# Optimization experiments

Hardware: AMD Instinct MI355X
Metric: run time of the kernel (lower is better)

## Reference

```python
import jax, jax.numpy as jnp
import numpy as np

D_MODEL = 512; D_STATE = 64; D_CONV = 4; EXPAND = 2; HEADDIM = 64
D_INNER = EXPAND * D_MODEL          # 1024
NHEADS = D_INNER // HEADDIM         # 16
D_IN_PROJ = 2 * D_INNER + 2 * D_STATE + NHEADS  # z, xBC, dt
CONV_DIM = D_INNER + 2 * D_STATE
BETA = 0.5
BATCH = 8; SEQLEN = 1024
EPS_LN = 1e-12; EPS_RMS = 1e-5


def layernorm(x, w, b, eps=EPS_LN):
    mu = jnp.mean(x, axis=-1, keepdims=True)
    var = jnp.var(x, axis=-1, keepdims=True)
    return (x - mu) * jax.lax.rsqrt(var + eps) * w + b


def causal_dw_conv(x, w, b):
    # x: (b, l, c); w: (c, d_conv) depthwise; causal left-pad d_conv-1
    xt = jnp.transpose(x, (0, 2, 1))                 # (b, c, l)
    k = w[:, None, :]                                # (c, 1, d_conv)
    y = jax.lax.conv_general_dilated(
        xt, k, window_strides=(1,), padding=[(D_CONV - 1, 0)],
        feature_group_count=CONV_DIM,
        dimension_numbers=('NCH', 'OIH', 'NCH'))
    return jnp.transpose(y, (0, 2, 1)) + b


def ssd(x, dt, A, Bm, Cm, Dp):
    # x: (b,l,h,p)  dt: (b,l,h)  A: (h)  Bm,Cm: (b,l,n)  Dp: (h)
    dA = jnp.exp(dt * A)  # (b,l,h) decay per step

    def step(h, inp):
        dA_t, dt_t, B_t, C_t, x_t = inp
        # h: (b, heads, p, n)
        h = h * dA_t[:, :, None, None] + jnp.einsum('bh,bn,bhp->bhpn', dt_t, B_t, x_t)
        y = jnp.einsum('bhpn,bn->bhp', h, C_t)
        return h, y

    init = jnp.zeros((x.shape[0], NHEADS, HEADDIM, D_STATE), x.dtype)
    xs = (jnp.moveaxis(dA, 1, 0), jnp.moveaxis(dt, 1, 0),
          jnp.moveaxis(Bm, 1, 0), jnp.moveaxis(Cm, 1, 0), jnp.moveaxis(x, 1, 0))
    _, ys = jax.lax.scan(step, init, xs)
    y = jnp.moveaxis(ys, 0, 1)           # (b,l,h,p)
    return y + x * Dp[None, None, :, None]


def mamba2(u, in_proj_w, conv_w, conv_b, dt_bias, A_log, Dp, norm_w, out_proj_w):
    zxbcdt = u @ in_proj_w.T                                   # (b,l,D_IN_PROJ)
    z, xBC, dt = jnp.split(zxbcdt, [D_INNER, D_INNER + CONV_DIM], axis=-1)
    dt = jax.nn.softplus(dt + dt_bias)                          # (b,l,h)
    xBC = jax.nn.silu(causal_dw_conv(xBC, conv_w, conv_b))
    x, Bm, Cm = jnp.split(xBC, [D_INNER, D_INNER + D_STATE], axis=-1)
    x = x.reshape(x.shape[0], x.shape[1], NHEADS, HEADDIM)
    A = -jnp.exp(A_log)
    y = ssd(x, dt, A, Bm, Cm, Dp)
    y = y.reshape(y.shape[0], y.shape[1], D_INNER)
    g = y * jax.nn.silu(z)                                      # gated RMSNorm
    g = g * jax.lax.rsqrt(jnp.mean(g * g, axis=-1, keepdims=True) + EPS_RMS) * norm_w
    return g @ out_proj_w.T


def ffn(x, w1, b1, w2, b2, lnw, lnb):
    h = jax.nn.gelu(x @ w1.T + b1, approximate=False)
    h = h @ w2.T + b2
    return layernorm(h + x, lnw, lnb)


def setup_inputs() -> dict:
    key = jax.random.key(0)
    ks = jax.random.split(key, 12)
    item_emb = jax.random.normal(ks[0], (BATCH, SEQLEN, D_MODEL), jnp.float32)
    item_idx = jnp.zeros((BATCH, SEQLEN), jnp.int32)          # single sequence per row
    flip_index = jnp.arange(SEQLEN - 1, -1, -1, dtype=jnp.int64)
    s = 0.02
    in_proj_w = jax.random.normal(ks[1], (D_IN_PROJ, D_MODEL), jnp.float32) * s
    conv_w = jax.random.uniform(ks[2], (CONV_DIM, D_CONV), jnp.float32, -0.5, 0.5)
    conv_b = jnp.zeros((CONV_DIM,), jnp.float32)
    # dt_bias = inverse softplus of dt ~ U[1e-3, 0.1] in log space (mamba init)
    dt = jnp.exp(jax.random.uniform(ks[3], (NHEADS,), jnp.float32,
                                    np.log(1e-3), np.log(0.1)))
    dt_bias = dt + jnp.log(-jnp.expm1(-dt))
    A_log = jnp.log(jax.random.uniform(ks[4], (NHEADS,), jnp.float32, 1.0, 16.0))
    Dp = jnp.ones((NHEADS,), jnp.float32)
    norm_w = jnp.ones((D_INNER,), jnp.float32)
    out_proj_w = jax.random.normal(ks[5], (D_MODEL, D_INNER), jnp.float32) * s
    ln_w = jnp.ones((D_MODEL,), jnp.float32); ln_b = jnp.zeros((D_MODEL,), jnp.float32)
    ffn_w1 = jax.random.normal(ks[6], (4 * D_MODEL, D_MODEL), jnp.float32) * s
    ffn_b1 = jnp.zeros((4 * D_MODEL,), jnp.float32)
    ffn_w2 = jax.random.normal(ks[7], (D_MODEL, 4 * D_MODEL), jnp.float32) * s
    ffn_b2 = jnp.zeros((D_MODEL,), jnp.float32)
    ffn_ln_w = jnp.ones((D_MODEL,), jnp.float32); ffn_ln_b = jnp.zeros((D_MODEL,), jnp.float32)
    return dict(item_emb=item_emb, item_idx=item_idx, flip_index=flip_index,
                in_proj_w=in_proj_w, conv_w=conv_w, conv_b=conv_b, dt_bias=dt_bias,
                A_log=A_log, Dp=Dp, norm_w=norm_w, out_proj_w=out_proj_w,
                ln_w=ln_w, ln_b=ln_b, ffn_w1=ffn_w1, ffn_b1=ffn_b1,
                ffn_w2=ffn_w2, ffn_b2=ffn_b2, ffn_ln_w=ffn_ln_w, ffn_ln_b=ffn_ln_b)


def reference(item_emb, item_idx, flip_index, in_proj_w, conv_w, conv_b, dt_bias,
              A_log, Dp, norm_w, out_proj_w, ln_w, ln_b,
              ffn_w1, ffn_b1, ffn_w2, ffn_b2, ffn_ln_w, ffn_ln_b):
    # item_idx (seq_idx) is all-zeros -> no state resets; dropout is eval-mode identity.
    params = (in_proj_w, conv_w, conv_b, dt_bias, A_log, Dp, norm_w, out_proj_w)
    fwd = mamba2(item_emb, *params)
    bwd = mamba2(item_emb[:, flip_index, :], *params)   # shared weights, as in source
    h = fwd + bwd * BETA + item_emb
    h = layernorm(h, ln_w, ln_b)
    return ffn(h, ffn_w1, ffn_b1, ffn_w2, ffn_b2, ffn_ln_w, ffn_ln_b)
```

## Files before the change

### kernel.cpp

```cpp
#include <hip/hip_runtime.h>
#include <math.h>

#define SEQ     1024
#define NBATCH  8
#define NTOK    8192
#define DMODEL  512
#define DINNER  1024
#define NHEADS  16
#define DPROJ   2192
#define DPROJP  2304
#define CONVDIM 1152
#define DFFN    2048

typedef short bf16x8 __attribute__((ext_vector_type(8)));
typedef float f32x4  __attribute__((ext_vector_type(4)));

__device__ inline unsigned short f2bf(float f) {
  union { float f; unsigned int u; } v; v.f = f;
  unsigned int u = v.u;
  return (unsigned short)((u + 0x7FFFu + ((u >> 16) & 1u)) >> 16);
}
__device__ inline float bf2f(unsigned short s) {
  union { unsigned int u; float f; } v; v.u = ((unsigned int)s) << 16;
  return v.f;
}

__device__ inline float fexp(float x) { return __expf(x); }
__device__ inline float frcp(float x) { return __builtin_amdgcn_rcpf(x); }
__device__ inline float silu_f(float v) { return v * frcp(1.f + fexp(-v)); }
__device__ inline float gelu_f(float v) {
  float x = v * 0.7071067811865476f;
  float ax = fabsf(x);
  float t = frcp(1.f + 0.3275911f * ax);
  float p = ((((1.061405429f * t - 1.453152027f) * t + 1.421413741f) * t
              - 0.284496736f) * t + 0.254829592f) * t;
  float er = copysignf(1.f - p * fexp(-ax * ax), x);
  return 0.5f * v * (1.f + er);
}

__device__ inline int xcd_swz(int flat, int nwg) {
  return (flat & 7) * (nwg >> 3) + (flat >> 3);
}

#define GLDS16(g, l)                                                         \
  __builtin_amdgcn_global_load_lds(                                          \
      (const __attribute__((address_space(1))) unsigned int*)(g),            \
      (__attribute__((address_space(3))) unsigned int*)(l), 16, 0, 0)

__global__ __launch_bounds__(256)
void cvt_all(const float* __restrict__ u, const float* __restrict__ inw,
             const float* __restrict__ outw, const float* __restrict__ w1,
             const float* __restrict__ w2,
             unsigned short* __restrict__ u_bf, unsigned short* __restrict__ winb,
             unsigned short* __restrict__ woutb, unsigned short* __restrict__ w1b,
             unsigned short* __restrict__ w2b) {
  int i = blockIdx.x * 256 + threadIdx.x;
  const int nu = NTOK * DMODEL;
  const int n0 = DPROJP * DMODEL;
  const int n1 = DMODEL * DINNER;
  const int n2 = DFFN * DMODEL;
  const int n3 = DMODEL * DFFN;
  if (i < nu) {
    u_bf[i] = f2bf(u[i]);
  } else if ((i -= nu) < n0) {
    int r = i / DMODEL;
    winb[i] = (r < DPROJ) ? f2bf(inw[i]) : (unsigned short)0;
  } else if ((i -= n0) < n1) {
    woutb[i] = f2bf(outw[i]);
  } else if ((i -= n1) < n2) {
    w1b[i] = f2bf(w1[i]);
  } else if ((i -= n2) < n3) {
    w2b[i] = f2bf(w2[i]);
  }
}

template <int MODE>
__global__ __launch_bounds__(256)
void gemm_bt(const unsigned short* __restrict__ A, const unsigned short* __restrict__ B,
             void* __restrict__ Cout, const float* __restrict__ bias,
             float* __restrict__ aux, int Ksub, int lda, int Nreal, size_t zstrideC) {
  __shared__ unsigned short sA[2][128 * 32];
  __shared__ unsigned short sB[2][128 * 32];
  const int tid = threadIdx.x;
  const int nwg = gridDim.x * gridDim.y * gridDim.z;
  const int flat = blockIdx.x + gridDim.x * (blockIdx.y + gridDim.y * blockIdx.z);
  const int swz = xcd_swz(flat, nwg);
  const int bx = swz % gridDim.x;
  const int tmp = swz / gridDim.x;
  const int by = tmp % gridDim.y;
  const int bz = tmp / gridDim.y;
  const int lane = tid & 63;
  const int wave = tid >> 6;
  const int wm = wave >> 1, wn = wave & 1;
  const int arow = tid >> 2;
  const int acol = (tid & 3) << 3;

  const unsigned short* pA = A + (size_t)(by * 128 + arow) * lda + bz * Ksub + acol;
  const unsigned short* pB = B + (size_t)(bx * 128 + arow) * lda + bz * Ksub + acol;
  const size_t stride64 = (size_t)64 * lda;
  char* sAw[2] = { (char*)&sA[0][0] + wave * 1024, (char*)&sA[1][0] + wave * 1024 };
  char* sBw[2] = { (char*)&sB[0][0] + wave * 1024, (char*)&sB[1][0] + wave * 1024 };

  f32x4 acc[4][4];
#pragma unroll
  for (int i = 0; i < 4; i++)
#pragma unroll
    for (int j = 0; j < 4; j++) { f32x4 z = {0.f, 0.f, 0.f, 0.f}; acc[i][j] = z; }

  GLDS16(pA, sAw[0]);
  GLDS16(pA + stride64, sAw[0] + 4096);
  GLDS16(pB, sBw[0]);
  GLDS16(pB + stride64, sBw[0] + 4096);
  pA += 32; pB += 32;
  __syncthreads();

  const int lrow = lane & 15;
  const int lkq = (lane >> 4) << 3;
  int cur = 0;
  for (int k0 = 0; k0 < Ksub; k0 += 32) {
    if (k0 + 32 < Ksub) {
      const int nxt = cur ^ 1;
      GLDS16(pA, sAw[nxt]);
      GLDS16(pA + stride64, sAw[nxt] + 4096);
      GLDS16(pB, sBw[nxt]);
      GLDS16(pB + stride64, sBw[nxt] + 4096);
      pA += 32; pB += 32;
    }
    bf16x8 af[4], bfr[4];
#pragma unroll
    for (int mi = 0; mi < 4; mi++)
      af[mi] = *(const bf16x8*)&sA[cur][(wm * 64 + mi * 16 + lrow) * 32 + lkq];
#pragma unroll
    for (int ni = 0; ni < 4; ni++)
      bfr[ni] = *(const bf16x8*)&sB[cur][(wn * 64 + ni * 16 + lrow) * 32 + lkq];
#pragma unroll
    for (int mi = 0; mi < 4; mi++)
#pragma unroll
      for (int ni = 0; ni < 4; ni++)
        acc[mi][ni] = __builtin_amdgcn_mfma_f32_16x16x32_bf16(af[mi], bfr[ni], acc[mi][ni], 0, 0, 0);
    __syncthreads();
    cur ^= 1;
  }

  const int row0 = by * 128 + wm * 64;
  const int col0 = bx * 128 + wn * 64;
  float* outf = (float*)Cout;
  unsigned short* outp16 = (unsigned short*)Cout + (size_t)bz * zstrideC;
#pragma unroll
  for (int mi = 0; mi < 4; mi++) {
#pragma unroll
    for (int ni = 0; ni < 4; ni++) {
      const int col = col0 + ni * 16 + lrow;
      if (col < Nreal) {
        const float bval = (MODE == 0 || MODE == 1) && bias ? bias[col] : 0.f;
#pragma unroll
        for (int r = 0; r < 4; r++) {
          const int row = row0 + mi * 16 + ((lane >> 4) << 2) + r;
          float v = acc[mi][ni][r] + bval;
          if (MODE == 1) {
            ((unsigned short*)Cout)[(size_t)row * Nreal + col] = f2bf(gelu_f(v));
          } else if (MODE == 2) {
            ((unsigned short*)Cout)[(size_t)row * Nreal + col] = f2bf(v);
            if (col >= 2176) aux[(size_t)row * 16 + (col - 2176)] = v;
          } else if (MODE == 3) {
            outp16[(size_t)row * Nreal + col] = f2bf(v);
          } else {
            outf[(size_t)row * Nreal + col] = v;
          }
        }
      }
    }
  }
}

__global__ __launch_bounds__(256)
void dt_conv_bc(const float* __restrict__ zdt, const float* __restrict__ dt_bias,
                float* __restrict__ dtf, float* __restrict__ dtb,
                const unsigned short* __restrict__ zxb, const float* __restrict__ cw,
                const float* __restrict__ cb,
                unsigned short* __restrict__ xbcf, unsigned short* __restrict__ xbcb) {
  const int tid = threadIdx.x;
  if (blockIdx.x < 1024) {
    int i = blockIdx.x * 256 + tid;
    int dir = i >> 17;
    int rem = i & 131071;
    int row = rem >> 10;
    int t = rem & 1023;
    int b = row >> 4, h = row & 15;
    int srow = (b << 10) + (dir ? (1023 - t) : t);
    float v = zdt[(size_t)srow * 16 + h] + dt_bias[h];
    float dt = (v > 20.f) ? v : log1pf(fexp(v));
    (dir ? dtb : dtf)[(row << 10) + t] = dt;
    return;
  }
  const int bid = blockIdx.x - 1024;
  const int sx = bid & 15, b = bid >> 4;
  const int c128 = tid & 127;
  const int c = 1024 + c128;
  const int seg = sx * 2 + (tid >> 7);
  const int t0 = seg << 5;
  const float w0 = cw[c * 4 + 0], w1 = cw[c * 4 + 1], w2 = cw[c * 4 + 2], w3 = cw[c * 4 + 3];
  const float bias = cb[c];
  const unsigned short* src = zxb + (size_t)(b << 10) * DPROJ + DINNER + c;
  unsigned short* dstf = xbcf + (size_t)(b << 10) * 128 + c128;
  unsigned short* dstb = xbcb + (size_t)(b << 10) * 128 + c128;
  float r0 = 0.f, r1 = 0.f, r2 = 0.f;
  if (t0 >= 3) {
    r0 = bf2f(src[(size_t)(t0 - 3) * DPROJ]);
    r1 = bf2f(src[(size_t)(t0 - 2) * DPROJ]);
    r2 = bf2f(src[(size_t)(t0 - 1) * DPROJ]);
  }
  for (int s = t0; s < t0 + 32; s++) {
    float x = bf2f(src[(size_t)s * DPROJ]);
    float vf = bias + w0 * r0 + w1 * r1 + w2 * r2 + w3 * x;
    dstf[(size_t)s * 128] = f2bf(silu_f(vf));
    int tp = 1026 - s;
    if (tp <= 1023) {
      float vb = bias + w0 * x + w1 * r2 + w2 * r1 + w3 * r0;
      dstb[(size_t)tp * 128] = f2bf(silu_f(vb));
    }
    r0 = r1; r1 = r2; r2 = x;
  }
  if (seg == 31) {
    float v2 = bias + w1 * r2 + w2 * r1 + w3 * r0;
    float v1 = bias + w2 * r2 + w3 * r1;
    float v0 = bias + w3 * r2;
    dstb[(size_t)2 * 128] = f2bf(silu_f(v2));
    dstb[(size_t)1 * 128] = f2bf(silu_f(v1));
    dstb[0] = f2bf(silu_f(v0));
  }
}

__global__ __launch_bounds__(512)
void ssd_chunk(const unsigned short* __restrict__ zxb,
               const unsigned short* __restrict__ xbcf, const unsigned short* __restrict__ xbcb,
               const float* __restrict__ cw, const float* __restrict__ cb,
               const float* __restrict__ dtf, const float* __restrict__ dtb,
               const float* __restrict__ A_log, const float* __restrict__ Dp,
               unsigned short* __restrict__ yf, unsigned short* __restrict__ yb) {
  const int blk = xcd_swz(blockIdx.x, 256);
  const int dir = blk >> 7;
  const int b = (blk >> 4) & 7;
  const int h = blk & 15;
  const unsigned short* xbc = dir ? xbcb : xbcf;
  const float* dts = (dir ? dtb : dtf) + ((size_t)((b << 4) + h) << 10);
  unsigned short* yo = dir ? yb : yf;
  const float A = -expf(A_log[h]);
  const float Dh = Dp[h];
  const int tid = threadIdx.x;
  const int lane = tid & 63;
  const int w = tid >> 6;
  const int wm = w >> 1;
  const int wn = w & 1;
  const int lrow = lane & 15;
  const int quad = lane >> 4;
  const int lk8 = quad << 3;
  const int bS = b << 10;

  __shared__ unsigned short Cb[2][64 * 72];
  __shared__ unsigned short Bb[2][64 * 72];
  __shared__ unsigned short Xt[2][64 * 72];
  __shared__ unsigned short Bt[2][64 * 72];
  __shared__ unsigned short Hb[2][64 * 72];
  __shared__ unsigned short Mb[64 * 72];
  __shared__ float sdt_all[1024];
  __shared__ float Lv_all[16][64];
  __shared__ float ev_all[16][64];
  __shared__ float wv_all[16][64];
  __shared__ float dtot_all[16];

  const unsigned short* bcrow = xbc + (size_t)(bS + (tid >> 3)) * 128 + (tid & 7) * 8;
  const int pr = tid & 31;
  const int sg = tid >> 5;
  const int ccx = h * 64 + pr * 2;
  const unsigned short* bvrow = xbc + (size_t)(bS + sg * 4) * 128 + pr * 2;
  const float4 wx0 = *(const float4*)(cw + ccx * 4);
  const float4 wx1 = *(const float4*)(cw + (ccx + 1) * 4);
  const float bx0 = cb[ccx], bx1 = cb[ccx + 1];

  uint4 vb, vc;
  unsigned int bv[4];
  unsigned int xin[7];

  auto stage_load = [&](int c) {
    const unsigned short* rp = bcrow + (size_t)c * 64 * 128;
    vb = *(const uint4*)(rp);
    vc = *(const uint4*)(rp + 64);
    const unsigned short* tp = bvrow + (size_t)c * 64 * 128;
#pragma unroll
    for (int k = 0; k < 4; k++) bv[k] = *(const unsigned int*)(tp + (size_t)k * 128);
    const int li0 = c * 64 + sg * 4 - 3;
#pragma unroll
    for (int j = 0; j < 7; j++) {
      const int li = li0 + j;
      const int g = dir ? (1023 - li) : li;
      xin[j] = (g >= 0 && g < 1024)
               ? *(const unsigned int*)(zxb + (size_t)(bS + g) * DPROJ + DINNER + ccx)
               : 0u;
    }
  };

  auto stage_write = [&](int buf, int c) {
    *(uint4*)&Bb[buf][(tid >> 3) * 72 + (tid & 7) * 8] = vb;
    *(uint4*)&Cb[buf][(tid >> 3) * 72 + (tid & 7) * 8] = vc;
    float f0[7], f1[7];
#pragma unroll
    for (int j = 0; j < 7; j++) {
      f0[j] = bf2f((unsigned short)(xin[j] & 0xffff));
      f1[j] = bf2f((unsigned short)(xin[j] >> 16));
    }
    unsigned short x0[4], x1[4], b0[4], b1[4];
#pragma unroll
    for (int k = 0; k < 4; k++) {
      const float ws = wv_all[c][sg * 4 + k];
      float v0 = bx0 + wx0.x * f0[k] + wx0.y * f0[k + 1] + wx0.z * f0[k + 2] + wx0.w * f0[k + 3];
      float v1 = bx1 + wx1.x * f1[k] + wx1.y * f1[k + 1] + wx1.z * f1[k + 2] + wx1.w * f1[k + 3];
      x0[k] = f2bf(silu_f(v0));
      x1[k] = f2bf(silu_f(v1));
      b0[k] = f2bf(bf2f((unsigned short)(bv[k] & 0xffff)) * ws);
      b1[k] = f2bf(bf2f((unsigned short)(bv[k] >> 16)) * ws);
    }
    *(uint2*)&Xt[buf][(pr * 2 + 0) * 72 + sg * 4] = *(const uint2*)x0;
    *(uint2*)&Xt[buf][(pr * 2 + 1) * 72 + sg * 4] = *(const uint2*)x1;
    *(uint2*)&Bt[buf][(pr * 2 + 0) * 72 + sg * 4] = *(const uint2*)b0;
    *(uint2*)&Bt[buf][(pr * 2 + 1) * 72 + sg * 4] = *(const uint2*)b1;
  };

  stage_load(0);

  *(float2*)&sdt_all[tid * 2] = *(const float2*)(dts + tid * 2);
  {
    uint4 z; z.x = 0u; z.y = 0u; z.z = 0u; z.w = 0u;
    *(uint4*)&Hb[0][(tid >> 3) * 72 + (tid & 7) * 8] = z;
  }
  __syncthreads();

#pragma unroll
  for (int r = 0; r < 2; r++) {
    const int c = w * 2 + r;
    float dtl = sdt_all[c * 64 + lane];
    float v = dtl;
#pragma unroll
    for (int off = 1; off < 64; off <<= 1) {
      float o = __shfl_up(v, off);
      if (lane >= off) v += o;
    }
    const float Lv = A * v;
    const float LL = __shfl(Lv, 63);
    Lv_all[c][lane] = Lv;
    ev_all[c][lane] = fexp(Lv);
    wv_all[c][lane] = dtl * fexp(LL - Lv);
    if (lane == 0) dtot_all[c] = fexp(LL);
  }
  __syncthreads();

  stage_write(0, 0);
  stage_load(1);
  __syncthreads();

  f32x4 hacc[2];
#pragma unroll
  for (int j = 0; j < 2; j++) { f32x4 z = {0.f, 0.f, 0.f, 0.f}; hacc[j] = z; }

  int cur = 0;
  for (int c = 0; c < 16; c++) {
    const int t0 = c << 6;

    f32x4 m1[2];
#pragma unroll
    for (int j = 0; j < 2; j++) { f32x4 z = {0.f, 0.f, 0.f, 0.f}; m1[j] = z; }
#pragma unroll
    for (int kq = 0; kq < 2; kq++) {
      bf16x8 af = *(const bf16x8*)&Cb[cur][(wm * 16 + lrow) * 72 + kq * 32 + lk8];
#pragma unroll
      for (int j = 0; j < 2; j++) {
        bf16x8 bf = *(const bf16x8*)&Bb[cur][(wn * 32 + j * 16 + lrow) * 72 + kq * 32 + lk8];
        m1[j] = __builtin_amdgcn_mfma_f32_16x16x32_bf16(af, bf, m1[j], 0, 0, 0);
      }
    }
#pragma unroll
    for (int r = 0; r < 4; r++) {
      const int i = wm * 16 + quad * 4 + r;
      const float Li = Lv_all[c][i];
#pragma unroll
      for (int j = 0; j < 2; j++) {
        const int s = wn * 32 + j * 16 + lrow;
        const float Ls = Lv_all[c][s];
        const float ds = sdt_all[c * 64 + s];
        float val = (s <= i) ? m1[j][r] * fexp(Li - Ls) * ds : 0.f;
        Mb[i * 72 + s] = f2bf(val);
      }
    }
    __syncthreads();

    f32x4 Y[2], T[2], S[2];
#pragma unroll
    for (int j = 0; j < 2; j++) {
      f32x4 z = {0.f, 0.f, 0.f, 0.f};
      Y[j] = z; T[j] = z; S[j] = z;
    }
#pragma unroll
    for (int kq = 0; kq < 2; kq++) {
      bf16x8 am = *(const bf16x8*)&Mb[(wm * 16 + lrow) * 72 + kq * 32 + lk8];
      bf16x8 ac = *(const bf16x8*)&Cb[cur][(wm * 16 + lrow) * 72 + kq * 32 + lk8];
      bf16x8 ax = *(const bf16x8*)&Xt[cur][(wm * 16 + lrow) * 72 + kq * 32 + lk8];
#pragma unroll
      for (int j = 0; j < 2; j++) {
        const int brow = (wn * 32 + j * 16 + lrow) * 72 + kq * 32 + lk8;
        bf16x8 bx = *(const bf16x8*)&Xt[cur][brow];
        bf16x8 bh = *(const bf16x8*)&Hb[cur][brow];
        bf16x8 bw = *(const bf16x8*)&Bt[cur][brow];
        Y[j] = __builtin_amdgcn_mfma_f32_16x16x32_bf16(am, bx, Y[j], 0, 0, 0);
        T[j] = __builtin_amdgcn_mfma_f32_16x16x32_bf16(ac, bh, T[j], 0, 0, 0);
        S[j] = __builtin_amdgcn_mfma_f32_16x16x32_bf16(ax, bw, S[j], 0, 0, 0);
      }
    }

    const float dtot = dtot_all[c];
#pragma unroll
    for (int r = 0; r < 4; r++) {
      const int i = wm * 16 + quad * 4 + r;
      const float ei = ev_all[c][i];
#pragma unroll
      for (int j = 0; j < 2; j++) {
        const int p = wn * 32 + j * 16 + lrow;
        float yv = Y[j][r] + ei * T[j][r] + Dh * bf2f(Xt[cur][p * 72 + i]);
        yo[(size_t)(bS + t0 + i) * DINNER + h * 64 + p] = f2bf(yv);
      }
    }
#pragma unroll
    for (int j = 0; j < 2; j++)
#pragma unroll
      for (int r = 0; r < 4; r++)
        hacc[j][r] = dtot * hacc[j][r] + S[j][r];

    const int nxt = cur ^ 1;
    if (c + 1 < 16) {
#pragma unroll
      for (int j = 0; j < 2; j++)
#pragma unroll
        for (int r = 0; r < 4; r++)
          Hb[nxt][(wm * 16 + quad * 4 + r) * 72 + wn * 32 + j * 16 + lrow] = f2bf(hacc[j][r]);
      stage_write(nxt, c + 1);
      if (c + 2 < 16) stage_load(c + 2);
    }
    __syncthreads();
    cur = nxt;
  }
}

__device__ inline float2 block_sum2_256(float a, float b) {
#pragma unroll
  for (int o = 32; o >= 1; o >>= 1) { a += __shfl_xor(a, o); b += __shfl_xor(b, o); }
  __shared__ float ra[4], rb[4];
  const int lane = threadIdx.x & 63, w = threadIdx.x >> 6;
  if (lane == 0) { ra[w] = a; rb[w] = b; }
  __syncthreads();
  float2 out;
  out.x = ra[0] + ra[1] + ra[2] + ra[3];
  out.y = rb[0] + rb[1] + rb[2] + rb[3];
  return out;
}

__global__ __launch_bounds__(256)
void gate_rms_comb(const unsigned short* __restrict__ yf, const unsigned short* __restrict__ yb,
                   const unsigned short* __restrict__ zxb, const float* __restrict__ nw,
                   unsigned short* __restrict__ comb) {
  const int bt = blockIdx.x;
  const int b = bt >> 10, t = bt & 1023;
  const int zrowb = (b << 10) + (1023 - t);
  const int tid = threadIdx.x;
  ushort4 yf4 = *(const ushort4*)(yf + (size_t)bt * DINNER + tid * 4);
  ushort4 yb4 = *(const ushort4*)(yb + (size_t)bt * DINNER + tid * 4);
  ushort4 zf4 = *(const ushort4*)(zxb + (size_t)bt * DPROJ + tid * 4);
  ushort4 zb4 = *(const ushort4*)(zxb + (size_t)zrowb * DPROJ + tid * 4);
  float gf[4], gb[4];
  gf[0] = bf2f(yf4.x) * silu_f(bf2f(zf4.x));
  gf[1] = bf2f(yf4.y) * silu_f(bf2f(zf4.y));
  gf[2] = bf2f(yf4.z) * silu_f(bf2f(zf4.z));
  gf[3] = bf2f(yf4.w) * silu_f(bf2f(zf4.w));
  gb[0] = bf2f(yb4.x) * silu_f(bf2f(zb4.x));
  gb[1] = bf2f(yb4.y) * silu_f(bf2f(zb4.y));
  gb[2] = bf2f(yb4.z) * silu_f(bf2f(zb4.z));
  gb[3] = bf2f(yb4.w) * silu_f(bf2f(zb4.w));
  float2 sr = block_sum2_256(gf[0]*gf[0] + gf[1]*gf[1] + gf[2]*gf[2] + gf[3]*gf[3],
                             gb[0]*gb[0] + gb[1]*gb[1] + gb[2]*gb[2] + gb[3]*gb[3]);
  float sf = rsqrtf(sr.x * (1.f / 1024.f) + 1e-5f);
  float sb = 0.5f * rsqrtf(sr.y * (1.f / 1024.f) + 1e-5f);
  float4 wv = *(const float4*)(nw + tid * 4);
  unsigned short* o = comb + (size_t)bt * DINNER + tid * 4;
  o[0] = f2bf((gf[0] * sf + gb[0] * sb) * wv.x);
  o[1] = f2bf((gf[1] * sf + gb[1] * sb) * wv.y);
  o[2] = f2bf((gf[2] * sf + gb[2] * sb) * wv.z);
  o[3] = f2bf((gf[3] * sf + gb[3] * sb) * wv.w);
}

__global__ __launch_bounds__(256)
void combine_ln(const unsigned short* __restrict__ mo, const float* __restrict__ u,
                const float* __restrict__ w, const float* __restrict__ bias,
                float* __restrict__ hln, unsigned short* __restrict__ hbf) {
  const int bt = blockIdx.x;
  const int tid = threadIdx.x;
  const float2 uu = *(const float2*)(u + (size_t)bt * DMODEL + tid * 2);
  float vx = uu.x, vy = uu.y;
#pragma unroll
  for (int z = 0; z < 2; z++) {
    ushort2 p = *(const ushort2*)(mo + (size_t)z * NTOK * DMODEL + (size_t)bt * DMODEL + tid * 2);
    vx += bf2f(p.x);
    vy += bf2f(p.y);
  }
  float2 sr = block_sum2_256(vx + vy, vx * vx + vy * vy);
  float mean = sr.x * (1.f / 512.f);
  float var = sr.y * (1.f / 512.f) - mean * mean;
  float inv = rsqrtf(var + 1e-12f);
  float2 wv = *(const float2*)(w + tid * 2);
  float2 bv = *(const float2*)(bias + tid * 2);
  float ox = (vx - mean) * inv * wv.x + bv.x;
  float oy = (vy - mean) * inv * wv.y + bv.y;
  *(float2*)(hln + (size_t)bt * DMODEL + tid * 2) = make_float2(ox, oy);
  hbf[(size_t)bt * DMODEL + tid * 2] = f2bf(ox);
  hbf[(size_t)bt * DMODEL + tid * 2 + 1] = f2bf(oy);
}

__global__ __launch_bounds__(256)
void final_ln(const unsigned short* __restrict__ f2, const float* __restrict__ b2,
              const float* __restrict__ hln,
              const float* __restrict__ w, const float* __restrict__ bias,
              float* __restrict__ outp) {
  const int bt = blockIdx.x;
  const int tid = threadIdx.x;
  const float2 bb = *(const float2*)(b2 + tid * 2);
  const float2 h = *(const float2*)(hln + (size_t)bt * DMODEL + tid * 2);
  float vx = bb.x + h.x;
  float vy = bb.y + h.y;
#pragma unroll
  for (int z = 0; z < 2; z++) {
    ushort2 p = *(const ushort2*)(f2 + (size_t)z * NTOK * DMODEL + (size_t)bt * DMODEL + tid * 2);
    vx += bf2f(p.x);
    vy += bf2f(p.y);
  }
  float2 sr = block_sum2_256(vx + vy, vx * vx + vy * vy);
  float mean = sr.x * (1.f / 512.f);
  float var = sr.y * (1.f / 512.f) - mean * mean;
  float inv = rsqrtf(var + 1e-12f);
  float2 wv = *(const float2*)(w + tid * 2);
  float2 bv = *(const float2*)(bias + tid * 2);
  *(float2*)(outp + (size_t)bt * DMODEL + tid * 2) =
      make_float2((vx - mean) * inv * wv.x + bv.x, (vy - mean) * inv * wv.y + bv.y);
}

extern "C" void kernel_launch(void* const* d_in, const int* in_sizes, int n_in,
                              void* d_out, int out_size, void* d_ws, size_t ws_size,
                              hipStream_t stream) {
  const float* item_emb   = (const float*)d_in[0];
  const float* in_proj_w  = (const float*)d_in[3];
  const float* conv_w     = (const float*)d_in[4];
  const float* conv_b     = (const float*)d_in[5];
  const float* dt_bias    = (const float*)d_in[6];
  const float* A_log      = (const float*)d_in[7];
  const float* Dp         = (const float*)d_in[8];
  const float* norm_w     = (const float*)d_in[9];
  const float* out_proj_w = (const float*)d_in[10];
  const float* ln_w       = (const float*)d_in[11];
  const float* ln_b       = (const float*)d_in[12];
  const float* w1         = (const float*)d_in[13];
  const float* b1         = (const float*)d_in[14];
  const float* w2         = (const float*)d_in[15];
  const float* b2         = (const float*)d_in[16];
  const float* fln_w      = (const float*)d_in[17];
  const float* fln_b      = (const float*)d_in[18];
  float* outp = (float*)d_out;
  char* ws = (char*)d_ws;

  const size_t o_ubf  = 0;
  const size_t o_win  = 8388608;
  const size_t o_wout = 10747904;
  const size_t o_w1   = 11796480;
  const size_t o_w2   = 13893632;
  const size_t o_dtf  = 15990784;
  const size_t o_dtb  = 16515072;
  const size_t o_zdt  = 17039360;
  const size_t o_zxb  = 17563648;
  const size_t o_xcf  = 53477376;
  const size_t o_xbcf = 72351744;
  const size_t o_xbcb = 74448896;
  const size_t o_yf   = 91226112;
  const size_t o_yb   = 108003328;
  const size_t o_comb = o_xcf;
  const size_t o_mo   = o_zxb;
  const size_t o_hln  = o_yb;
  const size_t o_hbf  = o_ubf;
  const size_t o_h1   = o_xbcf;
  const size_t o_f2   = o_zxb;

  unsigned short* u_bf  = (unsigned short*)(ws + o_ubf);
  unsigned short* winb  = (unsigned short*)(ws + o_win);
  unsigned short* woutb = (unsigned short*)(ws + o_wout);
  unsigned short* w1b   = (unsigned short*)(ws + o_w1);
  unsigned short* w2b   = (unsigned short*)(ws + o_w2);
  float* dtf = (float*)(ws + o_dtf);
  float* dtb = (float*)(ws + o_dtb);
  float* zdt = (float*)(ws + o_zdt);
  unsigned short* zxb  = (unsigned short*)(ws + o_zxb);
  unsigned short* xbcf = (unsigned short*)(ws + o_xbcf);
  unsigned short* xbcb = (unsigned short*)(ws + o_xbcb);
  unsigned short* yf  = (unsigned short*)(ws + o_yf);
  unsigned short* yb  = (unsigned short*)(ws + o_yb);
  unsigned short* comb = (unsigned short*)(ws + o_comb);
  unsigned short* mo  = (unsigned short*)(ws + o_mo);
  float* hln = (float*)(ws + o_hln);
  unsigned short* hbf = (unsigned short*)(ws + o_hbf);
  unsigned short* h1b = (unsigned short*)(ws + o_h1);
  unsigned short* f2  = (unsigned short*)(ws + o_f2);

  {
    int n = NTOK * DMODEL + DPROJP * DMODEL + DMODEL * DINNER + DFFN * DMODEL + DMODEL * DFFN;
    cvt_all<<<(n + 255) / 256, 256, 0, stream>>>(item_emb, in_proj_w, out_proj_w, w1, w2,
                                                 u_bf, winb, woutb, w1b, w2b);
  }

  gemm_bt<2><<<dim3(DPROJP / 128, NTOK / 128), 256, 0, stream>>>(
      u_bf, winb, zxb, nullptr, zdt, DMODEL, DMODEL, DPROJ, 0);

  dt_conv_bc<<<1152, 256, 0, stream>>>(zdt, dt_bias, dtf, dtb,
                                       zxb, conv_w, conv_b, xbcf, xbcb);

  ssd_chunk<<<256, 512, 0, stream>>>(zxb, xbcf, xbcb, conv_w, conv_b,
                                     dtf, dtb, A_log, Dp, yf, yb);

  gate_rms_comb<<<NTOK, 256, 0, stream>>>(yf, yb, zxb, norm_w, comb);

  gemm_bt<3><<<dim3(DMODEL / 128, NTOK / 128, 2), 256, 0, stream>>>(
      comb, woutb, mo, nullptr, nullptr, DINNER / 2, DINNER, DMODEL,
      (size_t)NTOK * DMODEL);

  combine_ln<<<NTOK, 256, 0, stream>>>(mo, item_emb, ln_w, ln_b, hln, hbf);

  gemm_bt<1><<<dim3(DFFN / 128, NTOK / 128), 256, 0, stream>>>(
      hbf, w1b, h1b, b1, nullptr, DMODEL, DMODEL, DFFN, 0);

  gemm_bt<3><<<dim3(DMODEL / 128, NTOK / 128, 2), 256, 0, stream>>>(
      h1b, w2b, f2, nullptr, nullptr, DFFN / 2, DFFN, DMODEL,
      (size_t)NTOK * DMODEL);

  final_ln<<<NTOK, 256, 0, stream>>>(f2, b2, hln, fln_w, fln_b, outp);

  (void)in_sizes; (void)n_in; (void)out_size; (void)ws_size;
}
```

Measured before the change: 320.8 us.

## Split SSD chunk kernel across headdim halves and load C/B fragments directly

Each (direction, batch, head) unit is now split into two blocks, one per 32-wide half of the head dimension, which doubles the grid to 512 blocks. The launch bounds request 4 blocks per CU so more work runs at once on the sequential chunk scan. The C and B MFMA fragments are now read straight from global memory into registers instead of being staged through shared memory. This shrinks shared memory use and removes some LDS traffic. In exchange, the C·B^T intra-chunk matrix and the per-chunk dt cumsum/B-weighting work are computed twice for each head, and the global fragment loads may add latency.

```diff
diff --git a/kernel.cpp b/kernel.cpp
--- a/kernel.cpp
+++ b/kernel.cpp
@@ -231,17 +231,19 @@
   }
 }
 
-__global__ __launch_bounds__(512)
+__global__ __launch_bounds__(512, 4)
 void ssd_chunk(const unsigned short* __restrict__ zxb,
                const unsigned short* __restrict__ xbcf, const unsigned short* __restrict__ xbcb,
                const float* __restrict__ cw, const float* __restrict__ cb,
                const float* __restrict__ dtf, const float* __restrict__ dtb,
                const float* __restrict__ A_log, const float* __restrict__ Dp,
                unsigned short* __restrict__ yf, unsigned short* __restrict__ yb) {
-  const int blk = xcd_swz(blockIdx.x, 256);
-  const int dir = blk >> 7;
-  const int b = (blk >> 4) & 7;
-  const int h = blk & 15;
+  const int blk = xcd_swz(blockIdx.x, 512);
+  const int ph = blk & 1;
+  const int unit = blk >> 1;
+  const int dir = unit >> 7;
+  const int b = (unit >> 4) & 7;
+  const int h = unit & 15;
   const unsigned short* xbc = dir ? xbcb : xbcf;
   const float* dts = (dir ? dtb : dtf) + ((size_t)((b << 4) + h) << 10);
   unsigned short* yo = dir ? yb : yf;
@@ -250,18 +252,16 @@
   const int tid = threadIdx.x;
   const int lane = tid & 63;
   const int w = tid >> 6;
-  const int wm = w >> 1;
-  const int wn = w & 1;
+  const int iw = w >> 1;
+  const int sw = w & 1;
   const int lrow = lane & 15;
   const int quad = lane >> 4;
   const int lk8 = quad << 3;
   const int bS = b << 10;
 
-  __shared__ unsigned short Cb[2][64 * 72];
-  __shared__ unsigned short Bb[2][64 * 72];
-  __shared__ unsigned short Xt[2][64 * 72];
+  __shared__ unsigned short Xt[2][32 * 72];
   __shared__ unsigned short Bt[2][64 * 72];
-  __shared__ unsigned short Hb[2][64 * 72];
+  __shared__ unsigned short Hb[2][32 * 72];
   __shared__ unsigned short Mb[64 * 72];
   __shared__ float sdt_all[1024];
   __shared__ float Lv_all[16][64];
@@ -269,29 +269,38 @@
   __shared__ float wv_all[16][64];
   __shared__ float dtot_all[16];
 
-  const unsigned short* bcrow = xbc + (size_t)(bS + (tid >> 3)) * 128 + (tid & 7) * 8;
   const int pr = tid & 31;
   const int sg = tid >> 5;
-  const int ccx = h * 64 + pr * 2;
   const unsigned short* bvrow = xbc + (size_t)(bS + sg * 4) * 128 + pr * 2;
+  const int pr2 = tid & 15;
+  const int sg2 = tid >> 4;
+  const int ccx = h * 64 + ph * 32 + pr2 * 2;
   const float4 wx0 = *(const float4*)(cw + ccx * 4);
   const float4 wx1 = *(const float4*)(cw + (ccx + 1) * 4);
   const float bx0 = cb[ccx], bx1 = cb[ccx + 1];
 
-  uint4 vb, vc;
   unsigned int bv[4];
-  unsigned int xin[7];
-
+  unsigned int xin[5];
+  bf16x8 af[2], bfr[4];
+
+  auto frag_load = [&](int c) {
+    const unsigned short* base = xbc + (size_t)(bS + c * 64) * 128;
+#pragma unroll
+    for (int kq = 0; kq < 2; kq++) {
+      af[kq] = *(const bf16x8*)(base + (size_t)(iw * 16 + lrow) * 128 + 64 + kq * 32 + lk8);
+#pragma unroll
+      for (int j = 0; j < 2; j++)
+        bfr[j * 2 + kq] =
+            *(const bf16x8*)(base + (size_t)(sw * 32 + j * 16 + lrow) * 128 + kq * 32 + lk8);
+    }
+  };
   auto stage_load = [&](int c) {
-    const unsigned short* rp = bcrow + (size_t)c * 64 * 128;
-    vb = *(const uint4*)(rp);
-    vc = *(const uint4*)(rp + 64);
     const unsigned short* tp = bvrow + (size_t)c * 64 * 128;
 #pragma unroll
     for (int k = 0; k < 4; k++) bv[k] = *(const unsigned int*)(tp + (size_t)k * 128);
-    const int li0 = c * 64 + sg * 4 - 3;
-#pragma unroll
-    for (int j = 0; j < 7; j++) {
+    const int li0 = c * 64 + sg2 * 2 - 3;
+#pragma unroll
+    for (int j = 0; j < 5; j++) {
       const int li = li0 + j;
       const int g = dir ? (1023 - li) : li;
       xin[j] = (g >= 0 && g < 1024)
@@ -299,39 +308,41 @@
                : 0u;
     }
   };
-
   auto stage_write = [&](int buf, int c) {
-    *(uint4*)&Bb[buf][(tid >> 3) * 72 + (tid & 7) * 8] = vb;
-    *(uint4*)&Cb[buf][(tid >> 3) * 72 + (tid & 7) * 8] = vc;
-    float f0[7], f1[7];
-#pragma unroll
-    for (int j = 0; j < 7; j++) {
+    unsigned short b0[4], b1[4];
+#pragma unroll
+    for (int k = 0; k < 4; k++) {
+      const float ws = wv_all[c][sg * 4 + k];
+      b0[k] = f2bf(bf2f((unsigned short)(bv[k] & 0xffff)) * ws);
+      b1[k] = f2bf(bf2f((unsigned short)(bv[k] >> 16)) * ws);
+    }
+    *(uint2*)&Bt[buf][(pr * 2 + 0) * 72 + sg * 4] = *(const uint2*)b0;
+    *(uint2*)&Bt[buf][(pr * 2 + 1) * 72 + sg * 4] = *(const uint2*)b1;
+    float f0[5], f1[5];
+#pragma unroll
+    for (int j = 0; j < 5; j++) {
       f0[j] = bf2f((unsigned short)(xin[j] & 0xffff));
       f1[j] = bf2f((unsigned short)(xin[j] >> 16));
     }
-    unsigned short x0[4], x1[4], b0[4], b1[4];
-#pragma unroll
-    for (int k = 0; k < 4; k++) {
-      const float ws = wv_all[c][sg * 4 + k];
+    unsigned short x0[2], x1[2];
+#pragma unroll
+    for (int k = 0; k < 2; k++) {
       float v0 = bx0 + wx0.x * f0[k] + wx0.y * f0[k + 1] + wx0.z * f0[k + 2] + wx0.w * f0[k + 3];
       float v1 = bx1 + wx1.x * f1[k] + wx1.y * f1[k + 1] + wx1.z * f1[k + 2] + wx1.w * f1[k + 3];
       x0[k] = f2bf(silu_f(v0));
       x1[k] = f2bf(silu_f(v1));
-      b0[k] = f2bf(bf2f((unsigned short)(bv[k] & 0xffff)) * ws);
-      b1[k] = f2bf(bf2f((unsigned short)(bv[k] >> 16)) * ws);
-    }
-    *(uint2*)&Xt[buf][(pr * 2 + 0) * 72 + sg * 4] = *(const uint2*)x0;
-    *(uint2*)&Xt[buf][(pr * 2 + 1) * 72 + sg * 4] = *(const uint2*)x1;
-    *(uint2*)&Bt[buf][(pr * 2 + 0) * 72 + sg * 4] = *(const uint2*)b0;
-    *(uint2*)&Bt[buf][(pr * 2 + 1) * 72 + sg * 4] = *(const uint2*)b1;
+    }
+    *(unsigned int*)&Xt[buf][(pr2 * 2 + 0) * 72 + sg2 * 2] = *(const unsigned int*)x0;
+    *(unsigned int*)&Xt[buf][(pr2 * 2 + 1) * 72 + sg2 * 2] = *(const unsigned int*)x1;
   };
 
+  frag_load(0);
   stage_load(0);
 
   *(float2*)&sdt_all[tid * 2] = *(const float2*)(dts + tid * 2);
-  {
+  if (tid < 288) {
     uint4 z; z.x = 0u; z.y = 0u; z.z = 0u; z.w = 0u;
-    *(uint4*)&Hb[0][(tid >> 3) * 72 + (tid & 7) * 8] = z;
+    *(uint4*)&Hb[0][tid * 8] = z;
   }
   __syncthreads();
 
@@ -358,9 +369,7 @@
   stage_load(1);
   __syncthreads();
 
-  f32x4 hacc[2];
-#pragma unroll
-  for (int j = 0; j < 2; j++) { f32x4 z = {0.f, 0.f, 0.f, 0.f}; hacc[j] = z; }
+  f32x4 hacc = {0.f, 0.f, 0.f, 0.f};
 
   int cur = 0;
   for (int c = 0; c < 16; c++) {
@@ -370,21 +379,17 @@
 #pragma unroll
     for (int j = 0; j < 2; j++) { f32x4 z = {0.f, 0.f, 0.f, 0.f}; m1[j] = z; }
 #pragma unroll
-    for (int kq = 0; kq < 2; kq++) {
-      bf16x8 af = *(const bf16x8*)&Cb[cur][(wm * 16 + lrow) * 72 + kq * 32 + lk8];
+    for (int kq = 0; kq < 2; kq++)
+#pragma unroll
+      for (int j = 0; j < 2; j++)
+        m1[j] = __builtin_amdgcn_mfma_f32_16x16x32_bf16(af[kq], bfr[j * 2 + kq], m1[j], 0, 0, 0);
+#pragma unroll
+    for (int r = 0; r < 4; r++) {
+      const int i = iw * 16 + quad * 4 + r;
+      const float Li = Lv_all[c][i];
 #pragma unroll
       for (int j = 0; j < 2; j++) {
-        bf16x8 bf = *(const bf16x8*)&Bb[cur][(wn * 32 + j * 16 + lrow) * 72 + kq * 32 + lk8];
-        m1[j] = __builtin_amdgcn_mfma_f32_16x16x32_bf16(af, bf, m1[j], 0, 0, 0);
-      }
-    }
-#pragma unroll
-    for (int r = 0; r < 4; r++) {
-      const int i = wm * 16 + quad * 4 + r;
-      const float Li = Lv_all[c][i];
-#pragma unroll
-      for (int j = 0; j < 2; j++) {
-        const int s = wn * 32 + j * 16 + lrow;
+        const int s = sw * 32 + j * 16 + lrow;
         const float Ls = Lv_all[c][s];
         const float ds = sdt_all[c * 64 + s];
         float val = (s <= i) ? m1[j][r] * fexp(Li - Ls) * ds : 0.f;
@@ -393,56 +398,45 @@
     }
     __syncthreads();
 
-    f32x4 Y[2], T[2], S[2];
-#pragma unroll
-    for (int j = 0; j < 2; j++) {
-      f32x4 z = {0.f, 0.f, 0.f, 0.f};
-      Y[j] = z; T[j] = z; S[j] = z;
-    }
+    f32x4 Y = {0.f, 0.f, 0.f, 0.f};
+    f32x4 T = {0.f, 0.f, 0.f, 0.f};
+    f32x4 S = {0.f, 0.f, 0.f, 0.f};
+    bf16x8 am[2], xp[2];
 #pragma unroll
     for (int kq = 0; kq < 2; kq++) {
-      bf16x8 am = *(const bf16x8*)&Mb[(wm * 16 + lrow) * 72 + kq * 32 + lk8];
-      bf16x8 ac = *(const bf16x8*)&Cb[cur][(wm * 16 + lrow) * 72 + kq * 32 + lk8];
-      bf16x8 ax = *(const bf16x8*)&Xt[cur][(wm * 16 + lrow) * 72 + kq * 32 + lk8];
-#pragma unroll
-      for (int j = 0; j < 2; j++) {
-        const int brow = (wn * 32 + j * 16 + lrow) * 72 + kq * 32 + lk8;
-        bf16x8 bx = *(const bf16x8*)&Xt[cur][brow];
-        bf16x8 bh = *(const bf16x8*)&Hb[cur][brow];
-        bf16x8 bw = *(const bf16x8*)&Bt[cur][brow];
-        Y[j] = __builtin_amdgcn_mfma_f32_16x16x32_bf16(am, bx, Y[j], 0, 0, 0);
-        T[j] = __builtin_amdgcn_mfma_f32_16x16x32_bf16(ac, bh, T[j], 0, 0, 0);
-        S[j] = __builtin_amdgcn_mfma_f32_16x16x32_bf16(ax, bw, S[j], 0, 0, 0);
-      }
+      am[kq] = *(const bf16x8*)&Mb[(iw * 16 + lrow) * 72 + kq * 32 + lk8];
+      xp[kq] = *(const bf16x8*)&Xt[cur][(sw * 16 + lrow) * 72 + kq * 32 + lk8];
+    }
+#pragma unroll
+    for (int kq = 0; kq < 2; kq++) {
+      bf16x8 bh = *(const bf16x8*)&Hb[cur][(sw * 16 + lrow) * 72 + kq * 32 + lk8];
+      bf16x8 bw = *(const bf16x8*)&Bt[cur][(iw * 16 + lrow) * 72 + kq * 32 + lk8];
+      Y = __builtin_amdgcn_mfma_f32_16x16x32_bf16(am[kq], xp[kq], Y, 0, 0, 0);
+      T = __builtin_amdgcn_mfma_f32_16x16x32_bf16(af[kq], bh, T, 0, 0, 0);
+      S = __builtin_amdgcn_mfma_f32_16x16x32_bf16(xp[kq], bw, S, 0, 0, 0);
     }
 
     const float dtot = dtot_all[c];
+    const int pl = sw * 16 + lrow;
 #pragma unroll
     for (int r = 0; r < 4; r++) {
-      const int i = wm * 16 + quad * 4 + r;
+      const int i = iw * 16 + quad * 4 + r;
       const float ei = ev_all[c][i];
-#pragma unroll
-      for (int j = 0; j < 2; j++) {
-        const int p = wn * 32 + j * 16 + lrow;
-        float yv = Y[j][r] + ei * T[j][r] + Dh * bf2f(Xt[cur][p * 72 + i]);
-        yo[(size_t)(bS + t0 + i) * DINNER + h * 64 + p] = f2bf(yv);
-      }
-    }
-#pragma unroll
-    for (int j = 0; j < 2; j++)
-#pragma unroll
-      for (int r = 0; r < 4; r++)
-        hacc[j][r] = dtot * hacc[j][r] + S[j][r];
+      float yv = Y[r] + ei * T[r] + Dh * bf2f(Xt[cur][pl * 72 + i]);
+      yo[(size_t)(bS + t0 + i) * DINNER + h * 64 + ph * 32 + pl] = f2bf(yv);
+    }
+#pragma unroll
+    for (int r = 0; r < 4; r++)
+      hacc[r] = dtot * hacc[r] + S[r];
 
     const int nxt = cur ^ 1;
     if (c + 1 < 16) {
 #pragma unroll
-      for (int j = 0; j < 2; j++)
-#pragma unroll
-        for (int r = 0; r < 4; r++)
-          Hb[nxt][(wm * 16 + quad * 4 + r) * 72 + wn * 32 + j * 16 + lrow] = f2bf(hacc[j][r]);
+      for (int r = 0; r < 4; r++)
+        Hb[nxt][(sw * 16 + quad * 4 + r) * 72 + iw * 16 + lrow] = f2bf(hacc[r]);
       stage_write(nxt, c + 1);
       if (c + 2 < 16) stage_load(c + 2);
+      frag_load(c + 1);
     }
     __syncthreads();
     cur = nxt;
@@ -625,7 +619,7 @@
   dt_conv_bc<<<1152, 256, 0, stream>>>(zdt, dt_bias, dtf, dtb,
                                        zxb, conv_w, conv_b, xbcf, xbcb);
 
-  ssd_chunk<<<256, 512, 0, stream>>>(zxb, xbcf, xbcb, conv_w, conv_b,
+  ssd_chunk<<<512, 512, 0, stream>>>(zxb, xbcf, xbcb, conv_w, conv_b,
                                      dtf, dtb, A_log, Dp, yf, yb);
 
   gate_rms_comb<<<NTOK, 256, 0, stream>>>(yf, yb, zxb, norm_w, comb);
```

Result: slower. 332.1 us (+3.5%).
